# Performance work log

Measured on AMD Instinct MI355X. Metric: run time of the kernel, lower is better.

Reference implementation:

```python
import jax, jax.numpy as jnp
import numpy as np

SENT_LEN, SENT_BATCH, WORD_LEN = 256, 64, 16
EMB, HID = 128, 256
CEMB, CHID = 64, 128
VOCAB, CVOCAB, TAGS = 50000, 128, 50


def setup_inputs() -> dict:
    key = jax.random.key(0)
    ks = jax.random.split(key, 14)
    s = 0.1  # param init scale, avoids gate saturation
    n = lambda k, shape: (jax.random.normal(k, shape, dtype=jnp.float32) * s)
    return {
        "sentences": jax.random.randint(ks[0], (SENT_LEN, SENT_BATCH), 0, VOCAB),
        "words": jax.random.randint(ks[1], (SENT_BATCH, WORD_LEN, SENT_LEN), 0, CVOCAB),
        "char_embedding_dim": CEMB,
        "char_hidden_dim": CHID,
        "word_emb": n(ks[2], (VOCAB, EMB)),
        "char_emb": n(ks[3], (CVOCAB, CEMB)),
        "Wih_c": n(ks[4], (4 * CHID, CEMB)),
        "Whh_c": n(ks[5], (4 * CHID, CHID)),
        "bih_c": n(ks[6], (4 * CHID,)),
        "bhh_c": n(ks[7], (4 * CHID,)),
        "Wih_w": n(ks[8], (4 * HID, EMB + CHID)),
        "Whh_w": n(ks[9], (4 * HID, HID)),
        "bih_w": n(ks[10], (4 * HID,)),
        "bhh_w": n(ks[11], (4 * HID,)),
        "W_tag": n(ks[12], (TAGS, HID)),
        "b_tag": n(ks[13], (TAGS,)),
    }


def _lstm_cell(h, c, x, Wih, Whh, b):
    # torch gate order: input, forget, cell(g), output
    gates = x @ Wih.T + h @ Whh.T + b
    i, f, g, o = jnp.split(gates, 4, axis=-1)
    c_new = jax.nn.sigmoid(f) * c + jax.nn.sigmoid(i) * jnp.tanh(g)
    h_new = jax.nn.sigmoid(o) * jnp.tanh(c_new)
    return h_new, c_new


def reference(sentences, words, char_embedding_dim, char_hidden_dim,
              word_emb, char_emb, Wih_c, Whh_c, bih_c, bhh_c,
              Wih_w, Whh_w, bih_w, bhh_w, W_tag, b_tag):
    sent_len, sent_batch = sentences.shape
    dt = word_emb.dtype

    embeds = word_emb[sentences]            # [T, B, EMB]
    ce = char_emb[words]                    # [B, WL, T, CEMB]

    # char LSTM: per sentence, seq=WL, batch=T; hidden carried ACROSS sentences
    b_c = bih_c + bhh_c

    def char_sentence(carry, sent_ce):      # sent_ce: [WL, T, CEMB]
        def step(hc, x):
            h, c = _lstm_cell(hc[0], hc[1], x, Wih_c, Whh_c, b_c)
            return (h, c), None
        carry, _ = jax.lax.scan(step, carry, sent_ce)
        return carry, carry[0]               # final h: [T, CHID]

    init_c = (jnp.zeros((sent_len, CHID), dt), jnp.zeros((sent_len, CHID), dt))
    _, char_finals = jax.lax.scan(char_sentence, init_c, ce)  # [B, T, CHID]
    char_finals = jnp.transpose(char_finals, (1, 0, 2))        # [T, B, CHID]

    x = jnp.concatenate([embeds, char_finals], axis=-1)        # [T, B, EMB+CHID]

    # word LSTM over time=T, batch=B
    b_w = bih_w + bhh_w

    def word_step(hc, xt):
        h, c = _lstm_cell(hc[0], hc[1], xt, Wih_w, Whh_w, b_w)
        return (h, c), h

    init_w = (jnp.zeros((sent_batch, HID), dt), jnp.zeros((sent_batch, HID), dt))
    _, lstm_out = jax.lax.scan(word_step, init_w, x)           # [T, B, HID]

    tag_space = lstm_out @ W_tag.T + b_tag                     # [T, B, TAGS]
    return jax.nn.log_softmax(tag_space, axis=-1)
```

## Files before the change

kernel.cpp:

```cpp
#include <hip/hip_runtime.h>
#include <hip/hip_bf16.h>
#include <cstdint>

#define SENT_LEN   256
#define SENT_BATCH 64
#define WORD_LEN   16
#define EMB        128
#define HID        256
#define CEMB       64
#define CHID       128
#define TAGS       50
#define K_IN       (EMB + CHID)
#define LOG2E      1.44269504f
#define N2LOG2E    -2.88539008f

typedef __attribute__((ext_vector_type(8))) short short8;
typedef __attribute__((ext_vector_type(4))) float f32x4;
typedef __attribute__((ext_vector_type(4))) int   i32x4;
typedef __attribute__((ext_vector_type(2))) long  lng2;

__device__ __forceinline__ float rcpf(float x) { return __builtin_amdgcn_rcpf(x); }
__device__ __forceinline__ float sig2(float xl) {
    return rcpf(1.f + __builtin_amdgcn_exp2f(-xl));
}
__device__ __forceinline__ float tanh2(float xl) {
    float e = __builtin_amdgcn_exp2f(-(xl + xl));
    return 2.f * rcpf(1.f + e) - 1.f;
}
__device__ __forceinline__ float lstm_act(float gi, float gf, float gg, float go, float& cst) {
    float c = sig2(gf) * cst + sig2(gi) * tanh2(gg);
    cst = c;
    float tc = 2.f * rcpf(1.f + __builtin_amdgcn_exp2f(N2LOG2E * c)) - 1.f;
    return sig2(go) * tc;
}
__device__ __forceinline__ float bf_lo(unsigned u) { return __uint_as_float(u << 16); }
__device__ __forceinline__ float bf_hi(unsigned u) { return __uint_as_float(u & 0xffff0000u); }
__device__ __forceinline__ unsigned short f2bfu(float f) {
    unsigned u = __float_as_uint(f);
    u += 0x7fff + ((u >> 16) & 1);
    return (unsigned short)(u >> 16);
}
__device__ __forceinline__ void block_sync_lds() {
    asm volatile("s_waitcnt lgkmcnt(0)\ns_barrier" ::: "memory");
}
__device__ __forceinline__ i32x4 mfma_i8_k64(lng2 a, lng2 b, i32x4 c) {
    c = __builtin_amdgcn_mfma_i32_16x16x32_i8(a.x, b.x, c, 0, 0, 0);
    return __builtin_amdgcn_mfma_i32_16x16x32_i8(a.y, b.y, c, 0, 0, 0);
}
template<int Q> __device__ __forceinline__ float qbcast(float x) {
    return __int_as_float(__builtin_amdgcn_mov_dpp(
        __float_as_int(x), Q * 0x55, 0xF, 0xF, false));
}

__global__ void prep_char(const float* __restrict__ Wih_c, const float* __restrict__ char_emb,
                          const float* __restrict__ bih_c, const float* __restrict__ bhh_c,
                          float* __restrict__ pre8) {
    int ch = blockIdx.x;
    int g  = threadIdx.x;
    float acc = bih_c[g] + bhh_c[g];
    const float* w = Wih_c + g * CEMB;
    const float* e = char_emb + ch * CEMB;
#pragma unroll
    for (int k = 0; k < CEMB; k++) acc += w[k] * e[k];
    int gt = g >> 7, j = g & 127;
    float s_e = (gt == 2) ? -2.f : -1.f;
    pre8[((ch * 128) + j) * 4 + gt] = acc * LOG2E * s_e;
}

__global__ void prep_wq(const float* __restrict__ Whh_w, const float* __restrict__ Wih_w,
                        signed char* __restrict__ wq, float* __restrict__ sw,
                        unsigned short* __restrict__ wihb) {
    int g = blockIdx.x;
    int lane = threadIdx.x;
    float4 v = reinterpret_cast<const float4*>(Whh_w + (size_t)g * HID)[lane];
    float m = fmaxf(fmaxf(fabsf(v.x), fabsf(v.y)), fmaxf(fabsf(v.z), fabsf(v.w)));
#pragma unroll
    for (int off = 32; off; off >>= 1) m = fmaxf(m, __shfl_xor(m, off, 64));
    m = fmaxf(m, 1e-20f);
    float inv = 127.f / m;
    int q0 = __float2int_rn(v.x * inv), q1 = __float2int_rn(v.y * inv);
    int q2 = __float2int_rn(v.z * inv), q3 = __float2int_rn(v.w * inv);
    int packed = (q0 & 255) | ((q1 & 255) << 8) | ((q2 & 255) << 16) | ((q3 & 255) << 24);
    reinterpret_cast<int*>(wq)[g * 64 + lane] = packed;
    if (lane == 0) sw[g] = m / 127.f;
    float4 wv = reinterpret_cast<const float4*>(Wih_w + (size_t)g * K_IN)[lane];
    uint2 p;
    p.x = (unsigned)f2bfu(wv.x) | ((unsigned)f2bfu(wv.y) << 16);
    p.y = (unsigned)f2bfu(wv.z) | ((unsigned)f2bfu(wv.w) << 16);
    reinterpret_cast<uint2*>(wihb + (size_t)g * K_IN)[lane] = p;
}

__global__ __launch_bounds__(512, 1) void char_lstm(
        const int* __restrict__ words, const float* __restrict__ Whh_c,
        const float* __restrict__ pre8, float* __restrict__ cf) {
    int t    = blockIdx.x;
    int tid  = threadIdx.x;
    int lane = tid & 63, w = tid >> 6;
    int nt   = lane & 3;
    int j    = w * 16 + (lane >> 2);
    int g    = nt * 128 + j;

    __shared__ __align__(16) signed char hv[2][128];

    const float4* wr = reinterpret_cast<const float4*>(Whh_c + (size_t)g * CHID);
    float mx = 1e-20f;
#pragma unroll
    for (int q = 0; q < 32; q++) {
        float4 f = wr[q];
        mx = fmaxf(mx, fmaxf(fmaxf(fabsf(f.x), fabsf(f.y)), fmaxf(fabsf(f.z), fabsf(f.w))));
    }
    float inv = 127.f / mx;
    int wqr[32];
#pragma unroll
    for (int q = 0; q < 32; q++) {
        float4 f = wr[q];
        wqr[q] = (__float2int_rn(f.x * inv) & 255)
               | ((__float2int_rn(f.y * inv) & 255) << 8)
               | ((__float2int_rn(f.z * inv) & 255) << 16)
               | ((__float2int_rn(f.w * inv) & 255) << 24);
    }
    float s_e   = (nt == 2) ? -2.f : -1.f;
    float swl_s = s_e * mx * (LOG2E / (127.f * 127.f));
    float m_a   = (nt == 2) ?  2.f :  1.f;
    float b_a   = (nt == 2) ? -1.f :  0.f;

    if (tid < 64) { reinterpret_cast<int*>(hv)[tid] = 0; }

    float cst = 0.f;
    int cid0 = words[t];
    int cid1 = words[SENT_LEN + t];
    float pl0 = pre8[(size_t)cid0 * 512 + tid];
    float pl1 = pre8[(size_t)cid1 * 512 + tid];
    int ci2 = words[2 * SENT_LEN + t];
    int ci3 = words[3 * SENT_LEN + t];
    __syncthreads();

    for (int u = 0; u < 512; u++) {
        float pf0 = pre8[(size_t)ci2 * 512 + tid];
        float pf1 = pre8[(size_t)ci3 * 512 + tid];
        ci2 = words[(((u << 1) + 4) & 1023) * SENT_LEN + t];
        ci3 = words[(((u << 1) + 5) & 1023) * SENT_LEN + t];

        {
            const i32x4* hp = reinterpret_cast<const i32x4*>(hv[0]);
            int a0 = 0, a1 = 0, a2 = 0, a3 = 0;
#pragma unroll
            for (int q = 0; q < 8; q++) {
                i32x4 hq = hp[q];
                a0 = __builtin_amdgcn_sdot4(hq.x, wqr[q * 4 + 0], a0, false);
                a1 = __builtin_amdgcn_sdot4(hq.y, wqr[q * 4 + 1], a1, false);
                a2 = __builtin_amdgcn_sdot4(hq.z, wqr[q * 4 + 2], a2, false);
                a3 = __builtin_amdgcn_sdot4(hq.w, wqr[q * 4 + 3], a3, false);
            }
            int s = (a0 + a1) + (a2 + a3);
            float e  = __builtin_amdgcn_exp2f(fmaf((float)s, swl_s, pl0));
            float av = m_a * rcpf(1.f + e) + b_a;
            float qi = qbcast<0>(av);
            float qf = qbcast<1>(av);
            float qg = qbcast<2>(av);
            float qo = qbcast<3>(av);
            float c  = fmaf(qf, cst, qi * qg);
            cst = c;
            float tc = 2.f * rcpf(1.f + __builtin_amdgcn_exp2f(N2LOG2E * c)) - 1.f;
            float h  = qo * tc;
            if (nt == 0)
                hv[1][j] = (signed char)__float2int_rn(h * 127.f);
            block_sync_lds();
        }
        {
            const i32x4* hp = reinterpret_cast<const i32x4*>(hv[1]);
            int a0 = 0, a1 = 0, a2 = 0, a3 = 0;
#pragma unroll
            for (int q = 0; q < 8; q++) {
                i32x4 hq = hp[q];
                a0 = __builtin_amdgcn_sdot4(hq.x, wqr[q * 4 + 0], a0, false);
                a1 = __builtin_amdgcn_sdot4(hq.y, wqr[q * 4 + 1], a1, false);
                a2 = __builtin_amdgcn_sdot4(hq.z, wqr[q * 4 + 2], a2, false);
                a3 = __builtin_amdgcn_sdot4(hq.w, wqr[q * 4 + 3], a3, false);
            }
            int s = (a0 + a1) + (a2 + a3);
            float e  = __builtin_amdgcn_exp2f(fmaf((float)s, swl_s, pl1));
            float av = m_a * rcpf(1.f + e) + b_a;
            float qi = qbcast<0>(av);
            float qf = qbcast<1>(av);
            float qg = qbcast<2>(av);
            float qo = qbcast<3>(av);
            float c  = fmaf(qf, cst, qi * qg);
            cst = c;
            float tc = 2.f * rcpf(1.f + __builtin_amdgcn_exp2f(N2LOG2E * c)) - 1.f;
            float h  = qo * tc;
            if (nt == 0) {
                hv[0][j] = (signed char)__float2int_rn(h * 127.f);
                if ((u & 7) == 7)
                    cf[((size_t)t * SENT_BATCH + (u >> 3)) * CHID + j] = h;
            }
            block_sync_lds();
        }
        pl0 = pf0; pl1 = pf1;
    }
}

#define XW_SEG 65
__global__ __launch_bounds__(256, 2) void xw_gemm(
        const int* __restrict__ sentences, const float* __restrict__ word_emb,
        const float* __restrict__ cf, const unsigned short* __restrict__ wihb,
        const float* __restrict__ bih_w, const float* __restrict__ bhh_w,
        uint2* __restrict__ xw8) {
    __shared__ short8 Apack[32 * XW_SEG];
    __shared__ short8 Bpack[32 * XW_SEG];
    __shared__ int sid_s[64];
    int tid = threadIdx.x;
    int j0 = blockIdx.x * 16;
    int row0 = blockIdx.y * 64;
    if (tid < 64) sid_s[tid] = sentences[row0 + tid];
    __syncthreads();

#pragma unroll
    for (int it = 0; it < 8; it++) {
        int idx = it * 256 + tid;
        int m = idx >> 5, k8 = idx & 31;
        int k = k8 * 8;
        int kt = k8 >> 2, lqs = k8 & 3;
        int lanes = (m & 15) + (lqs << 4);
        int seg = kt * 4 + (m >> 4);
        const float* asrc = (k < EMB)
            ? word_emb + (size_t)sid_s[m] * EMB + k
            : cf + (size_t)(row0 + m) * CHID + (k - EMB);
        float4 a0 = reinterpret_cast<const float4*>(asrc)[0];
        float4 a1 = reinterpret_cast<const float4*>(asrc)[1];
        short8 av;
        av[0] = (short)f2bfu(a0.x); av[1] = (short)f2bfu(a0.y);
        av[2] = (short)f2bfu(a0.z); av[3] = (short)f2bfu(a0.w);
        av[4] = (short)f2bfu(a1.x); av[5] = (short)f2bfu(a1.y);
        av[6] = (short)f2bfu(a1.z); av[7] = (short)f2bfu(a1.w);
        Apack[seg * XW_SEG + lanes] = av;
        const unsigned short* bsrc =
            wihb + (size_t)((m >> 4) * 256 + j0 + (m & 15)) * K_IN + k;
        Bpack[seg * XW_SEG + lanes] = *reinterpret_cast<const short8*>(bsrc);
    }
    __syncthreads();

    int lane = tid & 63, wv = tid >> 6, l15 = lane & 15, lq = lane >> 4;
    f32x4 acc[4] = {{0.f,0.f,0.f,0.f},{0.f,0.f,0.f,0.f},{0.f,0.f,0.f,0.f},{0.f,0.f,0.f,0.f}};
#pragma unroll
    for (int kt = 0; kt < 8; kt++) {
        short8 a = Apack[(kt * 4 + wv) * XW_SEG + lane];
#pragma unroll
        for (int nt = 0; nt < 4; nt++)
            acc[nt] = __builtin_amdgcn_mfma_f32_16x16x32_bf16(
                a, Bpack[(kt * 4 + nt) * XW_SEG + lane], acc[nt], 0, 0, 0);
    }
    float bb[4];
#pragma unroll
    for (int nt = 0; nt < 4; nt++)
        bb[nt] = bih_w[nt * 256 + j0 + l15] + bhh_w[nt * 256 + j0 + l15];
    int t = row0 >> 6;
#pragma unroll
    for (int r = 0; r < 4; r++) {
        int b = wv * 16 + lq * 4 + r;
        uint2 o;
        o.x = (unsigned)f2bfu((acc[0][r] + bb[0]) * LOG2E)
            | ((unsigned)f2bfu((acc[1][r] + bb[1]) * LOG2E) << 16);
        o.y = (unsigned)f2bfu((acc[2][r] + bb[2]) * LOG2E)
            | ((unsigned)f2bfu((acc[3][r] + bb[3]) * LOG2E) << 16);
        xw8[((size_t)b * SENT_LEN + t) * 256 + j0 + l15] = o;
    }
}

__global__ __launch_bounds__(1024, 1) void word_lstm(
        const uint2* __restrict__ xw8, const signed char* __restrict__ wq,
        const float* __restrict__ sw, float* __restrict__ h_out) {
    int b    = blockIdx.x;
    int tid  = threadIdx.x;
    int lane = tid & 63, w = tid >> 6;
    int l15  = lane & 15, lq = lane >> 4;
    int j    = w * 16 + l15;

    __shared__ __align__(16) signed char hv[2][256];

    lng2 bfr[4][4];
    float swl[4];
#pragma unroll
    for (int nt = 0; nt < 4; nt++) {
        int g = nt * 256 + j;
        swl[nt] = sw[g] * (LOG2E / 127.f);
#pragma unroll
        for (int kt = 0; kt < 4; kt++)
            bfr[nt][kt] = reinterpret_cast<const lng2*>(wq + (size_t)g * HID + kt * 64 + lq * 16)[0];
    }
    if (tid < 128) { reinterpret_cast<int*>(hv)[tid] = 0; }

    const uint2* xwb = xw8 + (size_t)b * SENT_LEN * 256;
    float cst = 0.f;
    uint2 xq0 = xwb[0 * 256 + j];
    uint2 xq1 = xwb[1 * 256 + j];
    uint2 xq2 = xwb[2 * 256 + j];
    uint2 xq3 = xwb[3 * 256 + j];
    __syncthreads();

    for (int u = 0; u < 128; u++) {
        uint2 xn0 = xwb[((((u << 1) + 4) & 255)) * 256 + j];
        uint2 xn1 = xwb[((((u << 1) + 5) & 255)) * 256 + j];

        {
            const lng2* hp = reinterpret_cast<const lng2*>(hv[0]);
            i32x4 acc[4] = {};
#pragma unroll
            for (int kt = 0; kt < 4; kt++) {
                lng2 a = hp[kt * 4 + lq];
#pragma unroll
                for (int nt = 0; nt < 4; nt++)
                    acc[nt] = mfma_i8_k64(a, bfr[nt][kt], acc[nt]);
            }
            float gi = (float)acc[0][0] * swl[0] + bf_lo(xq0.x);
            float gf = (float)acc[1][0] * swl[1] + bf_hi(xq0.x);
            float gg = (float)acc[2][0] * swl[2] + bf_lo(xq0.y);
            float go = (float)acc[3][0] * swl[3] + bf_hi(xq0.y);
            float h = lstm_act(gi, gf, gg, go, cst);
            if (lq == 0) {
                h_out[((size_t)(u << 1) * SENT_BATCH + b) * HID + j] = h;
                hv[1][j] = (signed char)__float2int_rn(h * 127.f);
            }
            block_sync_lds();
        }
        {
            const lng2* hp = reinterpret_cast<const lng2*>(hv[1]);
            i32x4 acc[4] = {};
#pragma unroll
            for (int kt = 0; kt < 4; kt++) {
                lng2 a = hp[kt * 4 + lq];
#pragma unroll
                for (int nt = 0; nt < 4; nt++)
                    acc[nt] = mfma_i8_k64(a, bfr[nt][kt], acc[nt]);
            }
            float gi = (float)acc[0][0] * swl[0] + bf_lo(xq1.x);
            float gf = (float)acc[1][0] * swl[1] + bf_hi(xq1.x);
            float gg = (float)acc[2][0] * swl[2] + bf_lo(xq1.y);
            float go = (float)acc[3][0] * swl[3] + bf_hi(xq1.y);
            float h = lstm_act(gi, gf, gg, go, cst);
            if (lq == 0) {
                h_out[((size_t)((u << 1) + 1) * SENT_BATCH + b) * HID + j] = h;
                hv[0][j] = (signed char)__float2int_rn(h * 127.f);
            }
            block_sync_lds();
        }
        xq0 = xq2; xq1 = xq3; xq2 = xn0; xq3 = xn1;
    }
}

__global__ __launch_bounds__(256) void tag_logsoftmax(
        const float* __restrict__ h_out, const float* __restrict__ W_tag,
        const float* __restrict__ b_tag, float* __restrict__ out) {
    __shared__ float wt_s[TAGS * 257];
    __shared__ float hr_s[8 * HID];
    int tid = threadIdx.x;
    int row0 = blockIdx.x * 8;
#pragma unroll 2
    for (int i = 0; i < TAGS; i++) wt_s[i * 257 + tid] = W_tag[i * HID + tid];
#pragma unroll
    for (int w = 0; w < 8; w++) hr_s[w * HID + tid] = h_out[(size_t)(row0 + w) * HID + tid];
    __syncthreads();

    int w4 = tid >> 6, l = tid & 63;
#pragma unroll
    for (int rep = 0; rep < 2; rep++) {
        int w = rep * 4 + w4;
        float acc = 0.f;
        if (l < TAGS) {
            acc = b_tag[l];
            const float* hr = hr_s + w * HID;
            const float* wr = wt_s + l * 257;
#pragma unroll 4
            for (int k = 0; k < HID; k++) acc += hr[k] * wr[k];
        }
        float m = (l < TAGS) ? acc : -1e30f;
#pragma unroll
        for (int off = 32; off; off >>= 1) m = fmaxf(m, __shfl_xor(m, off, 64));
        float e = (l < TAGS) ? __builtin_amdgcn_exp2f((acc - m) * LOG2E) : 0.f;
        float ssum = e;
#pragma unroll
        for (int off = 32; off; off >>= 1) ssum += __shfl_xor(ssum, off, 64);
        float lse = m + __logf(ssum);
        if (l < TAGS) out[(size_t)(row0 + w) * TAGS + l] = acc - lse;
    }
}

extern "C" void kernel_launch(void* const* d_in, const int* in_sizes, int n_in,
                              void* d_out, int out_size, void* d_ws, size_t ws_size,
                              hipStream_t stream) {
    (void)in_sizes; (void)n_in; (void)out_size; (void)ws_size;
    const int*   sentences = (const int*)d_in[0];
    const int*   words     = (const int*)d_in[1];
    const float* word_emb  = (const float*)d_in[4];
    const float* char_emb  = (const float*)d_in[5];
    const float* Wih_c     = (const float*)d_in[6];
    const float* Whh_c     = (const float*)d_in[7];
    const float* bih_c     = (const float*)d_in[8];
    const float* bhh_c     = (const float*)d_in[9];
    const float* Wih_w     = (const float*)d_in[10];
    const float* Whh_w     = (const float*)d_in[11];
    const float* bih_w     = (const float*)d_in[12];
    const float* bhh_w     = (const float*)d_in[13];
    const float* W_tag     = (const float*)d_in[14];
    const float* b_tag     = (const float*)d_in[15];
    float* out = (float*)d_out;

    char* ws = (char*)d_ws;
    size_t off = 0;
    float* pre8 = (float*)(ws + off);                 off += 128 * 512 * sizeof(float);
    signed char* wq = (signed char*)(ws + off);       off += 1024 * 256;
    float* sw = (float*)(ws + off);                   off += 1024 * sizeof(float);
    unsigned short* wihb = (unsigned short*)(ws + off); off += (size_t)1024 * K_IN * 2;
    off = (off + 255) & ~(size_t)255;
    float* cf = (float*)(ws + off);                   off += (size_t)SENT_LEN * SENT_BATCH * CHID * sizeof(float);
    uint2* xw8 = (uint2*)(ws + off);                  off += (size_t)SENT_LEN * SENT_BATCH * 256 * sizeof(uint2);
    float* h_out = (float*)(ws + off);                off += (size_t)SENT_LEN * SENT_BATCH * HID * sizeof(float);

    hipLaunchKernelGGL(prep_char, dim3(128), dim3(512), 0, stream,
                       Wih_c, char_emb, bih_c, bhh_c, pre8);
    hipLaunchKernelGGL(prep_wq, dim3(1024), dim3(64), 0, stream, Whh_w, Wih_w, wq, sw, wihb);
    hipLaunchKernelGGL(char_lstm, dim3(256), dim3(512), 0, stream,
                       words, Whh_c, pre8, cf);
    hipLaunchKernelGGL(xw_gemm, dim3(16, 256), dim3(256), 0, stream,
                       sentences, word_emb, cf, wihb, bih_w, bhh_w, xw8);
    hipLaunchKernelGGL(word_lstm, dim3(SENT_BATCH), dim3(1024), 0, stream,
                       xw8, wq, sw, h_out);
    hipLaunchKernelGGL(tag_logsoftmax, dim3((SENT_LEN * SENT_BATCH) / 8), dim3(256), 0, stream,
                       h_out, W_tag, b_tag, out);
}
```

Before: 955.1 us.

## Fuse input-projection GEMM into char LSTM epilogue, keep char features in LDS

Removes the separate xw_gemm kernel. Each char_lstm block now stages its time step's word embeddings and final char hidden states as bf16 in shared memory, then runs the x·Wih MFMA GEMM itself at the end and writes xw8 directly. This drops the cf global round-trip and one kernel launch. In exchange, B fragments are read straight from global memory by each block without LDS staging, and only 256 blocks do the GEMM work at the tail of the serial char LSTM.

```diff
diff --git a/kernel.cpp b/kernel.cpp
--- a/kernel.cpp
+++ b/kernel.cpp
@@ -92,7 +92,10 @@
 
 __global__ __launch_bounds__(512, 1) void char_lstm(
         const int* __restrict__ words, const float* __restrict__ Whh_c,
-        const float* __restrict__ pre8, float* __restrict__ cf) {
+        const float* __restrict__ pre8, const int* __restrict__ sentences,
+        const float* __restrict__ word_emb, const unsigned short* __restrict__ wihb,
+        const float* __restrict__ bih_w, const float* __restrict__ bhh_w,
+        uint2* __restrict__ xw8) {
     int t    = blockIdx.x;
     int tid  = threadIdx.x;
     int lane = tid & 63, w = tid >> 6;
@@ -101,6 +104,7 @@
     int g    = nt * 128 + j;
 
     __shared__ __align__(16) signed char hv[2][128];
+    __shared__ __align__(16) unsigned short xls[64][264];
 
     const float4* wr = reinterpret_cast<const float4*>(Whh_c + (size_t)g * CHID);
     float mx = 1e-20f;
@@ -123,6 +127,26 @@
     float swl_s = s_e * mx * (LOG2E / (127.f * 127.f));
     float m_a   = (nt == 2) ?  2.f :  1.f;
     float b_a   = (nt == 2) ? -1.f :  0.f;
+
+    {
+        int b  = tid >> 3;
+        int c8 = tid & 7;
+        int sid = sentences[t * 64 + b];
+        const float4* ep = reinterpret_cast<const float4*>(
+            word_emb + (size_t)sid * EMB + c8 * 16);
+        float4 e0 = ep[0], e1 = ep[1], e2 = ep[2], e3 = ep[3];
+        short8 v0, v1;
+        v0[0] = (short)f2bfu(e0.x); v0[1] = (short)f2bfu(e0.y);
+        v0[2] = (short)f2bfu(e0.z); v0[3] = (short)f2bfu(e0.w);
+        v0[4] = (short)f2bfu(e1.x); v0[5] = (short)f2bfu(e1.y);
+        v0[6] = (short)f2bfu(e1.z); v0[7] = (short)f2bfu(e1.w);
+        v1[0] = (short)f2bfu(e2.x); v1[1] = (short)f2bfu(e2.y);
+        v1[2] = (short)f2bfu(e2.z); v1[3] = (short)f2bfu(e2.w);
+        v1[4] = (short)f2bfu(e3.x); v1[5] = (short)f2bfu(e3.y);
+        v1[6] = (short)f2bfu(e3.z); v1[7] = (short)f2bfu(e3.w);
+        *reinterpret_cast<short8*>(&xls[b][c8 * 16])     = v0;
+        *reinterpret_cast<short8*>(&xls[b][c8 * 16 + 8]) = v1;
+    }
 
     if (tid < 64) { reinterpret_cast<int*>(hv)[tid] = 0; }
 
@@ -192,78 +216,50 @@
             if (nt == 0) {
                 hv[0][j] = (signed char)__float2int_rn(h * 127.f);
                 if ((u & 7) == 7)
-                    cf[((size_t)t * SENT_BATCH + (u >> 3)) * CHID + j] = h;
+                    xls[u >> 3][128 + j] = f2bfu(h);
             }
             block_sync_lds();
         }
         pl0 = pf0; pl1 = pf1;
     }
-}
-
-#define XW_SEG 65
-__global__ __launch_bounds__(256, 2) void xw_gemm(
-        const int* __restrict__ sentences, const float* __restrict__ word_emb,
-        const float* __restrict__ cf, const unsigned short* __restrict__ wihb,
-        const float* __restrict__ bih_w, const float* __restrict__ bhh_w,
-        uint2* __restrict__ xw8) {
-    __shared__ short8 Apack[32 * XW_SEG];
-    __shared__ short8 Bpack[32 * XW_SEG];
-    __shared__ int sid_s[64];
-    int tid = threadIdx.x;
-    int j0 = blockIdx.x * 16;
-    int row0 = blockIdx.y * 64;
-    if (tid < 64) sid_s[tid] = sentences[row0 + tid];
-    __syncthreads();
-
-#pragma unroll
-    for (int it = 0; it < 8; it++) {
-        int idx = it * 256 + tid;
-        int m = idx >> 5, k8 = idx & 31;
-        int k = k8 * 8;
-        int kt = k8 >> 2, lqs = k8 & 3;
-        int lanes = (m & 15) + (lqs << 4);
-        int seg = kt * 4 + (m >> 4);
-        const float* asrc = (k < EMB)
-            ? word_emb + (size_t)sid_s[m] * EMB + k
-            : cf + (size_t)(row0 + m) * CHID + (k - EMB);
-        float4 a0 = reinterpret_cast<const float4*>(asrc)[0];
-        float4 a1 = reinterpret_cast<const float4*>(asrc)[1];
-        short8 av;
-        av[0] = (short)f2bfu(a0.x); av[1] = (short)f2bfu(a0.y);
-        av[2] = (short)f2bfu(a0.z); av[3] = (short)f2bfu(a0.w);
-        av[4] = (short)f2bfu(a1.x); av[5] = (short)f2bfu(a1.y);
-        av[6] = (short)f2bfu(a1.z); av[7] = (short)f2bfu(a1.w);
-        Apack[seg * XW_SEG + lanes] = av;
-        const unsigned short* bsrc =
-            wihb + (size_t)((m >> 4) * 256 + j0 + (m & 15)) * K_IN + k;
-        Bpack[seg * XW_SEG + lanes] = *reinterpret_cast<const short8*>(bsrc);
-    }
-    __syncthreads();
-
-    int lane = tid & 63, wv = tid >> 6, l15 = lane & 15, lq = lane >> 4;
-    f32x4 acc[4] = {{0.f,0.f,0.f,0.f},{0.f,0.f,0.f,0.f},{0.f,0.f,0.f,0.f},{0.f,0.f,0.f,0.f}};
-#pragma unroll
-    for (int kt = 0; kt < 8; kt++) {
-        short8 a = Apack[(kt * 4 + wv) * XW_SEG + lane];
-#pragma unroll
-        for (int nt = 0; nt < 4; nt++)
-            acc[nt] = __builtin_amdgcn_mfma_f32_16x16x32_bf16(
-                a, Bpack[(kt * 4 + nt) * XW_SEG + lane], acc[nt], 0, 0, 0);
-    }
-    float bb[4];
-#pragma unroll
-    for (int nt = 0; nt < 4; nt++)
-        bb[nt] = bih_w[nt * 256 + j0 + l15] + bhh_w[nt * 256 + j0 + l15];
-    int t = row0 >> 6;
-#pragma unroll
-    for (int r = 0; r < 4; r++) {
-        int b = wv * 16 + lq * 4 + r;
-        uint2 o;
-        o.x = (unsigned)f2bfu((acc[0][r] + bb[0]) * LOG2E)
-            | ((unsigned)f2bfu((acc[1][r] + bb[1]) * LOG2E) << 16);
-        o.y = (unsigned)f2bfu((acc[2][r] + bb[2]) * LOG2E)
-            | ((unsigned)f2bfu((acc[3][r] + bb[3]) * LOG2E) << 16);
-        xw8[((size_t)b * SENT_LEN + t) * 256 + j0 + l15] = o;
+
+    {
+        int l15 = lane & 15, lq = lane >> 4;
+        int mt  = w & 3;
+        short8 af[8];
+#pragma unroll
+        for (int kt = 0; kt < 8; kt++)
+            af[kt] = *reinterpret_cast<const short8*>(&xls[mt * 16 + l15][kt * 32 + lq * 8]);
+#pragma unroll 1
+        for (int jt = (w >> 2); jt < 16; jt += 2) {
+            int j0 = jt * 16;
+            f32x4 acc[4] = {{0.f,0.f,0.f,0.f},{0.f,0.f,0.f,0.f},
+                            {0.f,0.f,0.f,0.f},{0.f,0.f,0.f,0.f}};
+#pragma unroll
+            for (int kt = 0; kt < 8; kt++) {
+#pragma unroll
+                for (int n2 = 0; n2 < 4; n2++) {
+                    short8 bf = *reinterpret_cast<const short8*>(
+                        wihb + (size_t)(n2 * 256 + j0 + l15) * K_IN + kt * 32 + lq * 8);
+                    acc[n2] = __builtin_amdgcn_mfma_f32_16x16x32_bf16(
+                        af[kt], bf, acc[n2], 0, 0, 0);
+                }
+            }
+            float bb[4];
+#pragma unroll
+            for (int n2 = 0; n2 < 4; n2++)
+                bb[n2] = bih_w[n2 * 256 + j0 + l15] + bhh_w[n2 * 256 + j0 + l15];
+#pragma unroll
+            for (int r = 0; r < 4; r++) {
+                int br = mt * 16 + lq * 4 + r;
+                uint2 o;
+                o.x = (unsigned)f2bfu((acc[0][r] + bb[0]) * LOG2E)
+                    | ((unsigned)f2bfu((acc[1][r] + bb[1]) * LOG2E) << 16);
+                o.y = (unsigned)f2bfu((acc[2][r] + bb[2]) * LOG2E)
+                    | ((unsigned)f2bfu((acc[3][r] + bb[3]) * LOG2E) << 16);
+                xw8[((size_t)br * SENT_LEN + t) * 256 + j0 + l15] = o;
+            }
+        }
     }
 }
 
@@ -412,7 +408,6 @@
     float* sw = (float*)(ws + off);                   off += 1024 * sizeof(float);
     unsigned short* wihb = (unsigned short*)(ws + off); off += (size_t)1024 * K_IN * 2;
     off = (off + 255) & ~(size_t)255;
-    float* cf = (float*)(ws + off);                   off += (size_t)SENT_LEN * SENT_BATCH * CHID * sizeof(float);
     uint2* xw8 = (uint2*)(ws + off);                  off += (size_t)SENT_LEN * SENT_BATCH * 256 * sizeof(uint2);
     float* h_out = (float*)(ws + off);                off += (size_t)SENT_LEN * SENT_BATCH * HID * sizeof(float);
 
@@ -420,9 +415,7 @@
                        Wih_c, char_emb, bih_c, bhh_c, pre8);
     hipLaunchKernelGGL(prep_wq, dim3(1024), dim3(64), 0, stream, Whh_w, Wih_w, wq, sw, wihb);
     hipLaunchKernelGGL(char_lstm, dim3(256), dim3(512), 0, stream,
-                       words, Whh_c, pre8, cf);
-    hipLaunchKernelGGL(xw_gemm, dim3(16, 256), dim3(256), 0, stream,
-                       sentences, word_emb, cf, wihb, bih_w, bhh_w, xw8);
+                       words, Whh_c, pre8, sentences, word_emb, wihb, bih_w, bhh_w, xw8);
     hipLaunchKernelGGL(word_lstm, dim3(SENT_BATCH), dim3(1024), 0, stream,
                        xw8, wq, sw, h_out);
     hipLaunchKernelGGL(tag_logsoftmax, dim3((SENT_LEN * SENT_BATCH) / 8), dim3(256), 0, stream,
```

After: 945.3 us. No clear change (-1.0%).
